# Optimization experiments

Hardware: AMD Instinct MI355X
Metric: run time of the kernel (lower is better)

## Reference

```python
import jax, jax.numpy as jnp
import numpy as np

N, E, F_IN = 100000, 1000000, 128
H, C = 4, 32
HC = H * C
D_DIR = 128
G = 250
HID, CLS = 128, 2
ALPHA = 0.5
NEG = 0.2  # LeakyReLU slope in GATv2


def setup_inputs() -> dict:
    key = jax.random.key(0)
    ks = jax.random.split(key, 16)
    p = lambda k, shape: 0.02 * jax.random.normal(k, shape, jnp.float32)
    return {
        "x": jax.random.normal(ks[0], (N, F_IN), jnp.float32),
        "edge_index": jax.random.randint(ks[1], (2, E), 0, N, dtype=jnp.int32),
        "edge_attr": jax.random.normal(ks[2], (E, 1), jnp.float32),
        "batch": jnp.sort(jax.random.randint(ks[3], (N,), 0, G, dtype=jnp.int32)),
        "dir_w_in": p(ks[4], (2, F_IN, D_DIR)),
        "dir_b_in": jnp.zeros((2, D_DIR), jnp.float32),
        "dir_w_out": p(ks[5], (2, F_IN, D_DIR)),
        "dir_b_out": jnp.zeros((2, D_DIR), jnp.float32),
        "gat_wl": p(ks[6], (F_IN, HC)),
        "gat_wr": p(ks[7], (F_IN, HC)),
        "gat_we": p(ks[8], (1, HC)),
        "gat_att": p(ks[9], (H, C)),
        "gat_b": jnp.zeros((HC,), jnp.float32),
        "w1": p(ks[10], (D_DIR + HC, HID)),
        "b1": jnp.zeros((HID,), jnp.float32),
        "w2": p(ks[11], (HID, CLS)),
        "b2": jnp.zeros((CLS,), jnp.float32),
    }


def _gcn(x, src, dst, W, b):
    # GCNConv with add_self_loops=False (forced by DirGNNConv), unit edge weights.
    deg = jnp.zeros((N,), x.dtype).at[dst].add(1.0)
    dinv = jnp.where(deg > 0, 1.0 / jnp.sqrt(jnp.maximum(deg, 1.0)), 0.0)
    norm = dinv[src] * dinv[dst]  # [E]
    h = x @ W  # [N, D]
    out = jnp.zeros((N, W.shape[1]), x.dtype).at[dst].add(norm[:, None] * h[src])
    return out + b


def _mean_pool(h, batch):
    cnt = jnp.zeros((G,), h.dtype).at[batch].add(1.0)
    s = jnp.zeros((G, h.shape[1]), h.dtype).at[batch].add(h)
    return s / jnp.maximum(cnt, 1.0)[:, None]


def _forward(x, edge_index, edge_attr, batch, dir_w_in, dir_b_in, dir_w_out, dir_b_out,
             gat_wl, gat_wr, gat_we, gat_att, gat_b, w1, b1, w2, b2):
    src, dst = edge_index[0], edge_index[1]
    # --- DirGNN branch: alpha * GCN(flipped edges) + (1-alpha) * GCN(edges), relu between ---
    h = x
    for i in range(2):
        x_in = _gcn(h, src, dst, dir_w_in[i], dir_b_in[i])
        x_out = _gcn(h, dst, src, dir_w_out[i], dir_b_out[i])
        h = jax.nn.relu(ALPHA * x_out + (1.0 - ALPHA) * x_in)
    x1 = _mean_pool(h, batch)  # [G, D_DIR]
    # --- GATv2 branch (self loops appended, edge_attr fill value 1.0) ---
    loop = jnp.arange(N, dtype=src.dtype)
    s2 = jnp.concatenate([src, loop])
    d2 = jnp.concatenate([dst, loop])
    ea = jnp.concatenate([edge_attr, jnp.ones((N, 1), edge_attr.dtype)], axis=0)
    gl = (x @ gat_wl).reshape(N, H, C)  # source transform
    gr = (x @ gat_wr).reshape(N, H, C)  # target transform
    ee = (ea @ gat_we).reshape(-1, H, C)
    e = jax.nn.leaky_relu(gl[s2] + gr[d2] + ee, NEG)  # [E+N, H, C]
    logits = jnp.einsum('ehc,hc->eh', e, gat_att)
    # segment softmax over incoming edges of each target node (self loops => nonempty)
    m = jnp.full((N, H), -jnp.inf, logits.dtype).at[d2].max(logits)
    ex = jnp.exp(logits - m[d2])
    denom = jnp.zeros((N, H), logits.dtype).at[d2].add(ex)
    att = ex / denom[d2]
    out2 = jnp.zeros((N, H, C), x.dtype).at[d2].add(att[:, :, None] * gl[s2])
    x2 = _mean_pool(out2.reshape(N, HC) + gat_b, batch)  # [G, HC]
    # --- head ---
    z = jnp.concatenate([x1, x2], axis=1)
    z = jax.nn.relu(z @ w1 + b1)
    return z @ w2 + b2  # [G, CLS]


def reference(x, edge_index, edge_attr, batch, dir_w_in, dir_b_in, dir_w_out, dir_b_out,
              gat_wl, gat_wr, gat_we, gat_att, gat_b, w1, b1, w2, b2):
    return _forward(x, edge_index, edge_attr, batch, dir_w_in, dir_b_in, dir_w_out, dir_b_out,
                    gat_wl, gat_wr, gat_we, gat_att, gat_b, w1, b1, w2, b2)
```

## Files before the change

kernel.cpp:

```cpp
#include <hip/hip_runtime.h>
#include <cstdint>

#define FDIM 128
#define PCH 64

static inline int cdiv(long long a, long long b) { return (int)((a + b - 1) / b); }

__global__ __launch_bounds__(256) void degi_kernel(const int* __restrict__ src,
                                                   const int* __restrict__ dst,
                                                   int* __restrict__ deg_in,
                                                   int* __restrict__ deg_out, int E) {
  int base = (blockIdx.x * 256 + threadIdx.x) * 2;
  if (base + 2 <= E) {
    int2 s2 = *(const int2*)(src + base);
    int2 d2 = *(const int2*)(dst + base);
    atomicAdd(&deg_in[d2.x], 1);
    atomicAdd(&deg_in[d2.y], 1);
    atomicAdd(&deg_out[s2.x], 1);
    atomicAdd(&deg_out[s2.y], 1);
  } else {
    for (int i = base; i < E; i++) {
      atomicAdd(&deg_in[dst[i]], 1);
      atomicAdd(&deg_out[src[i]], 1);
    }
  }
}

__global__ __launch_bounds__(256) void dinv2_kernel(const int* __restrict__ degs,
                                                    float* __restrict__ dinv, int n2) {
  int i = blockIdx.x * 256 + threadIdx.x;
  if (i < n2) {
    int v = degs[i];
    dinv[i] = v > 0 ? 1.0f / sqrtf((float)v) : 0.f;
  }
}

__global__ __launch_bounds__(256) void cnt_sorted(const int* __restrict__ batch,
                                                  float* __restrict__ cnt, int N, int G) {
  int g = blockIdx.x * 256 + threadIdx.x;
  if (g >= G) return;
  int lo = 0, hi = N;
  while (lo < hi) { int mid = (lo + hi) >> 1; if (batch[mid] < g) lo = mid + 1; else hi = mid; }
  int lo2 = lo, hi2 = N;
  while (lo2 < hi2) { int mid = (lo2 + hi2) >> 1; if (batch[mid] <= g) lo2 = mid + 1; else hi2 = mid; }
  cnt[g] = (float)(lo2 - lo);
}

__global__ __launch_bounds__(256) void scan1(const int* __restrict__ in, int* __restrict__ out,
                                             int* __restrict__ bsums, int n) {
  __shared__ int tmp[256];
  int t = threadIdx.x;
  int base = blockIdx.x * 1024 + t * 4;
  int a[4];
#pragma unroll
  for (int j = 0; j < 4; j++) a[j] = (base + j < n) ? in[base + j] : 0;
  int s = a[0] + a[1] + a[2] + a[3];
  tmp[t] = s;
  __syncthreads();
  for (int off = 1; off < 256; off <<= 1) {
    int v = (t >= off) ? tmp[t - off] : 0;
    __syncthreads();
    tmp[t] += v;
    __syncthreads();
  }
  int excl = tmp[t] - s;
  int run = excl;
#pragma unroll
  for (int j = 0; j < 4; j++) {
    if (base + j < n) out[base + j] = run;
    run += a[j];
  }
  if (t == 255) bsums[blockIdx.x] = tmp[255];
}

__global__ __launch_bounds__(256) void scan2(const int* __restrict__ bsums,
                                             int* __restrict__ boff, int nb) {
  __shared__ int tmp[256];
  int t = threadIdx.x;
  int s = (t < nb) ? bsums[t] : 0;
  tmp[t] = s;
  __syncthreads();
  for (int off = 1; off < 256; off <<= 1) {
    int v = (t >= off) ? tmp[t - off] : 0;
    __syncthreads();
    tmp[t] += v;
    __syncthreads();
  }
  if (t < nb) boff[t] = tmp[t] - s;
}

__global__ __launch_bounds__(256) void scan3(const int* __restrict__ scanned,
                                             const int* __restrict__ boff,
                                             int* __restrict__ rp_in, int* __restrict__ cur_in,
                                             int* __restrict__ rp_out, int* __restrict__ cur_out,
                                             int N, int E, int n2) {
  int i = blockIdx.x * 256 + threadIdx.x;
  if (i < n2) {
    int v = scanned[i] + boff[i >> 10];
    if (i < N) { rp_in[i] = v; cur_in[i] = v; }
    else { v -= E; rp_out[i - N] = v; cur_out[i - N] = v; }
  }
}

__global__ __launch_bounds__(256) void mm0_fill(const float* __restrict__ A,
                                                const float* __restrict__ W0,
                                                const float* __restrict__ W1,
                                                float* __restrict__ out0,
                                                float* __restrict__ out1, int nrows, int mmB,
                                                const int* __restrict__ src,
                                                const int* __restrict__ dst,
                                                const float* __restrict__ eattr,
                                                int* __restrict__ cur_in,
                                                int* __restrict__ cur_out,
                                                int2* __restrict__ csr_in,
                                                int* __restrict__ csr_out_dst, int E, int fillB) {
  __shared__ float As[64][128];
  __shared__ float Ws[64][64];
  int T = mmB + fillB;
  int bid = blockIdx.x;
  int tid = threadIdx.x;
  long long f0 = (long long)bid * fillB / T;
  long long f1 = (long long)(bid + 1) * fillB / T;

  if (f1 > f0) {
    int base = ((int)f0 * 256 + tid) * 4;
    if (base + 4 <= E) {
      int4 s4 = *(const int4*)(src + base);
      int4 d4 = *(const int4*)(dst + base);
      float4 e4 = *(const float4*)(eattr + base);
      int p0 = atomicAdd(&cur_in[d4.x], 1);
      int p1 = atomicAdd(&cur_in[d4.y], 1);
      int p2 = atomicAdd(&cur_in[d4.z], 1);
      int p3 = atomicAdd(&cur_in[d4.w], 1);
      int q0 = atomicAdd(&cur_out[s4.x], 1);
      int q1 = atomicAdd(&cur_out[s4.y], 1);
      int q2 = atomicAdd(&cur_out[s4.z], 1);
      int q3 = atomicAdd(&cur_out[s4.w], 1);
      csr_in[p0] = make_int2(s4.x, __float_as_int(e4.x));
      csr_in[p1] = make_int2(s4.y, __float_as_int(e4.y));
      csr_in[p2] = make_int2(s4.z, __float_as_int(e4.z));
      csr_in[p3] = make_int2(s4.w, __float_as_int(e4.w));
      csr_out_dst[q0] = d4.x;
      csr_out_dst[q1] = d4.y;
      csr_out_dst[q2] = d4.z;
      csr_out_dst[q3] = d4.w;
    } else {
      for (int i = base; i < E; i++) {
        int s = src[i], d = dst[i];
        int p = atomicAdd(&cur_in[d], 1);
        csr_in[p] = make_int2(s, __float_as_int(eattr[i]));
        int q = atomicAdd(&cur_out[s], 1);
        csr_out_dst[q] = d;
      }
    }
    return;
  }

  int mb = bid - (int)f0;
  int r0 = mb * 64;

#pragma unroll
  for (int i = 0; i < 8; i++) {
    int v = tid + 256 * i;
    int r = v >> 5, k4 = (v & 31) << 2;
    int row = r0 + r;
    float4 a;
    if (row < nrows) a = *(const float4*)(A + (size_t)row * FDIM + k4);
    else a = make_float4(0.f, 0.f, 0.f, 0.f);
    int swz = ((r >> 2) & 7) << 2;
    *(float4*)(&As[r][k4 ^ swz]) = a;
  }

  int tx = tid & 15, ty = tid >> 4;
  int rbase = ty * 4;
  int swz = (ty & 7) << 2;

  for (int p = 0; p < 4; p++) {
    const float* W = (p < 2) ? W0 : W1;
    float* out = (p < 2) ? out0 : out1;
    int cb = (p & 1) * 64;
    float acc[4][4] = {};

    for (int kh = 0; kh < 2; kh++) {
      __syncthreads();
#pragma unroll
      for (int i = 0; i < 4; i++) {
        int v = tid + 256 * i;
        int k = v >> 4, c4 = (v & 15) << 2;
        *(float4*)(&Ws[k][c4]) = *(const float4*)(W + (kh * 64 + k) * FDIM + cb + c4);
      }
      __syncthreads();

#pragma unroll 8
      for (int k = 0; k < 64; k++) {
        int kx = (kh * 64 + k) ^ swz;
        float a0 = As[rbase + 0][kx];
        float a1 = As[rbase + 1][kx];
        float a2 = As[rbase + 2][kx];
        float a3 = As[rbase + 3][kx];
        float4 w = *(float4*)(&Ws[k][tx * 4]);
        acc[0][0] += a0 * w.x; acc[0][1] += a0 * w.y; acc[0][2] += a0 * w.z; acc[0][3] += a0 * w.w;
        acc[1][0] += a1 * w.x; acc[1][1] += a1 * w.y; acc[1][2] += a1 * w.z; acc[1][3] += a1 * w.w;
        acc[2][0] += a2 * w.x; acc[2][1] += a2 * w.y; acc[2][2] += a2 * w.z; acc[2][3] += a2 * w.w;
        acc[3][0] += a3 * w.x; acc[3][1] += a3 * w.y; acc[3][2] += a3 * w.z; acc[3][3] += a3 * w.w;
      }
    }

#pragma unroll
    for (int rr = 0; rr < 4; rr++) {
      int row = r0 + rbase + rr;
      if (row < nrows) {
        float4 o = make_float4(acc[rr][0], acc[rr][1], acc[rr][2], acc[rr][3]);
        *(float4*)(out + (size_t)row * FDIM + cb + tx * 4) = o;
      }
    }
  }
}

__global__ __launch_bounds__(256) void mm128d(const float* __restrict__ A,
                                              const float* __restrict__ W0,
                                              const float* __restrict__ W1,
                                              float* __restrict__ out0,
                                              float* __restrict__ out1, int nrows) {
  __shared__ float As[64][128];
  __shared__ float Ws[64][64];
  int r0 = blockIdx.x * 64;
  int tid = threadIdx.x;

#pragma unroll
  for (int i = 0; i < 8; i++) {
    int v = tid + 256 * i;
    int r = v >> 5, k4 = (v & 31) << 2;
    int row = r0 + r;
    float4 a;
    if (row < nrows) a = *(const float4*)(A + (size_t)row * FDIM + k4);
    else a = make_float4(0.f, 0.f, 0.f, 0.f);
    int swz = ((r >> 2) & 7) << 2;
    *(float4*)(&As[r][k4 ^ swz]) = a;
  }

  int tx = tid & 15, ty = tid >> 4;
  int rbase = ty * 4;
  int swz = (ty & 7) << 2;

  for (int p = 0; p < 4; p++) {
    const float* W = (p < 2) ? W0 : W1;
    float* out = (p < 2) ? out0 : out1;
    int cb = (p & 1) * 64;
    float acc[4][4] = {};

    for (int kh = 0; kh < 2; kh++) {
      __syncthreads();
#pragma unroll
      for (int i = 0; i < 4; i++) {
        int v = tid + 256 * i;
        int k = v >> 4, c4 = (v & 15) << 2;
        *(float4*)(&Ws[k][c4]) = *(const float4*)(W + (kh * 64 + k) * FDIM + cb + c4);
      }
      __syncthreads();

#pragma unroll 8
      for (int k = 0; k < 64; k++) {
        int kx = (kh * 64 + k) ^ swz;
        float a0 = As[rbase + 0][kx];
        float a1 = As[rbase + 1][kx];
        float a2 = As[rbase + 2][kx];
        float a3 = As[rbase + 3][kx];
        float4 w = *(float4*)(&Ws[k][tx * 4]);
        acc[0][0] += a0 * w.x; acc[0][1] += a0 * w.y; acc[0][2] += a0 * w.z; acc[0][3] += a0 * w.w;
        acc[1][0] += a1 * w.x; acc[1][1] += a1 * w.y; acc[1][2] += a1 * w.z; acc[1][3] += a1 * w.w;
        acc[2][0] += a2 * w.x; acc[2][1] += a2 * w.y; acc[2][2] += a2 * w.z; acc[2][3] += a2 * w.w;
        acc[3][0] += a3 * w.x; acc[3][1] += a3 * w.y; acc[3][2] += a3 * w.z; acc[3][3] += a3 * w.w;
      }
    }

#pragma unroll
    for (int rr = 0; rr < 4; rr++) {
      int row = r0 + rbase + rr;
      if (row < nrows) {
        float4 o = make_float4(acc[rr][0], acc[rr][1], acc[rr][2], acc[rr][3]);
        *(float4*)(out + (size_t)row * FDIM + cb + tx * 4) = o;
      }
    }
  }
}

__global__ __launch_bounds__(128) void gcn_gather4(const float4* __restrict__ tin,
                                                   const float4* __restrict__ tout,
                                                   const int* __restrict__ rp_in,
                                                   const int* __restrict__ deg_in,
                                                   const int2* __restrict__ adj_in,
                                                   const int* __restrict__ rp_out,
                                                   const int* __restrict__ deg_out,
                                                   const int* __restrict__ adj_out,
                                                   const float* __restrict__ dinv_in,
                                                   const float* __restrict__ dinv_out,
                                                   const float* __restrict__ bin,
                                                   const float* __restrict__ bout,
                                                   float4* __restrict__ outp, int N) {
  int grp = threadIdx.x >> 5, lane = threadIdx.x & 31;
  int d = blockIdx.x * 4 + grp;
  if (d >= N) return;
  float wi = 0.5f * dinv_in[d], wo = 0.5f * dinv_out[d];
  float4 a0 = make_float4(0.f, 0.f, 0.f, 0.f);
  float4 a1 = a0, a2 = a0, a3 = a0;

  int p = rp_in[d], n1 = deg_in[d];
  int k = 0;
  for (; k + 4 <= n1; k += 4) {
    int s0 = adj_in[p + k].x, s1 = adj_in[p + k + 1].x, s2 = adj_in[p + k + 2].x, s3 = adj_in[p + k + 3].x;
    float w0 = wi * dinv_in[s0], w1 = wi * dinv_in[s1], w2 = wi * dinv_in[s2], w3 = wi * dinv_in[s3];
    float4 v0 = tin[(size_t)s0 * 32 + lane];
    float4 v1 = tin[(size_t)s1 * 32 + lane];
    float4 v2 = tin[(size_t)s2 * 32 + lane];
    float4 v3 = tin[(size_t)s3 * 32 + lane];
    a0.x += w0 * v0.x; a0.y += w0 * v0.y; a0.z += w0 * v0.z; a0.w += w0 * v0.w;
    a1.x += w1 * v1.x; a1.y += w1 * v1.y; a1.z += w1 * v1.z; a1.w += w1 * v1.w;
    a2.x += w2 * v2.x; a2.y += w2 * v2.y; a2.z += w2 * v2.z; a2.w += w2 * v2.w;
    a3.x += w3 * v3.x; a3.y += w3 * v3.y; a3.z += w3 * v3.z; a3.w += w3 * v3.w;
  }
  for (; k < n1; k++) {
    int s = adj_in[p + k].x;
    float w = wi * dinv_in[s];
    float4 v = tin[(size_t)s * 32 + lane];
    a0.x += w * v.x; a0.y += w * v.y; a0.z += w * v.z; a0.w += w * v.w;
  }

  int q = rp_out[d], n2 = deg_out[d];
  k = 0;
  for (; k + 4 <= n2; k += 4) {
    int s0 = adj_out[q + k], s1 = adj_out[q + k + 1], s2 = adj_out[q + k + 2], s3 = adj_out[q + k + 3];
    float w0 = wo * dinv_out[s0], w1 = wo * dinv_out[s1], w2 = wo * dinv_out[s2], w3 = wo * dinv_out[s3];
    float4 v0 = tout[(size_t)s0 * 32 + lane];
    float4 v1 = tout[(size_t)s1 * 32 + lane];
    float4 v2 = tout[(size_t)s2 * 32 + lane];
    float4 v3 = tout[(size_t)s3 * 32 + lane];
    a0.x += w0 * v0.x; a0.y += w0 * v0.y; a0.z += w0 * v0.z; a0.w += w0 * v0.w;
    a1.x += w1 * v1.x; a1.y += w1 * v1.y; a1.z += w1 * v1.z; a1.w += w1 * v1.w;
    a2.x += w2 * v2.x; a2.y += w2 * v2.y; a2.z += w2 * v2.z; a2.w += w2 * v2.w;
    a3.x += w3 * v3.x; a3.y += w3 * v3.y; a3.z += w3 * v3.z; a3.w += w3 * v3.w;
  }
  for (; k < n2; k++) {
    int s = adj_out[q + k];
    float w = wo * dinv_out[s];
    float4 v = tout[(size_t)s * 32 + lane];
    a0.x += w * v.x; a0.y += w * v.y; a0.z += w * v.z; a0.w += w * v.w;
  }

  float4 acc;
  acc.x = (a0.x + a1.x) + (a2.x + a3.x);
  acc.y = (a0.y + a1.y) + (a2.y + a3.y);
  acc.z = (a0.z + a1.z) + (a2.z + a3.z);
  acc.w = (a0.w + a1.w) + (a2.w + a3.w);

  const float4* b1 = (const float4*)bin;
  const float4* b2 = (const float4*)bout;
  float4 ba = b1[lane], bb = b2[lane];
  float4 o;
  o.x = acc.x + 0.5f * (ba.x + bb.x);
  o.y = acc.y + 0.5f * (ba.y + bb.y);
  o.z = acc.z + 0.5f * (ba.z + bb.z);
  o.w = acc.w + 0.5f * (ba.w + bb.w);
  o.x = o.x > 0.f ? o.x : 0.f;
  o.y = o.y > 0.f ? o.y : 0.f;
  o.z = o.z > 0.f ? o.z : 0.f;
  o.w = o.w > 0.f ? o.w : 0.f;
  outp[(size_t)d * 32 + lane] = o;
}

__global__ __launch_bounds__(128) void gat_fused2(const float4* __restrict__ gl,
                                                  const float4* __restrict__ gr,
                                                  const int* __restrict__ rp,
                                                  const int* __restrict__ deg,
                                                  const int2* __restrict__ adj,
                                                  const float* __restrict__ we,
                                                  const float* __restrict__ att,
                                                  const float* __restrict__ gatb,
                                                  float4* __restrict__ outp, int N) {
  int grp = threadIdx.x >> 5, lane = threadIdx.x & 31;
  int d = blockIdx.x * 4 + grp;
  if (d >= N) return;

  float4 grv = gr[(size_t)d * 32 + lane];
  float4 wev = ((const float4*)we)[lane];
  float4 atv = ((const float4*)att)[lane];

  int p = rp[d], n1 = deg[d];
  float m = -1e30f, den = 0.f;
  float4 o = make_float4(0.f, 0.f, 0.f, 0.f);

#define GAT_LOGIT(g4, ea, pv)                                                     \
  {                                                                               \
    float vx = g4.x + grv.x + (ea) * wev.x; vx = vx > 0.f ? vx : 0.2f * vx;       \
    float vy = g4.y + grv.y + (ea) * wev.y; vy = vy > 0.f ? vy : 0.2f * vy;       \
    float vz = g4.z + grv.z + (ea) * wev.z; vz = vz > 0.f ? vz : 0.2f * vz;       \
    float vw = g4.w + grv.w + (ea) * wev.w; vw = vw > 0.f ? vw : 0.2f * vw;       \
    pv = vx * atv.x + vy * atv.y + vz * atv.z + vw * atv.w;                       \
    pv += __shfl_xor(pv, 1);                                                      \
    pv += __shfl_xor(pv, 2);                                                      \
    pv += __shfl_xor(pv, 4);                                                      \
  }

#define GAT_UPDATE(g4, pv)                                                        \
  {                                                                               \
    float mn = fmaxf(m, pv);                                                      \
    float sc = expf(m - mn);                                                      \
    float w = expf(pv - mn);                                                      \
    den = den * sc + w;                                                           \
    o.x = o.x * sc + w * g4.x;                                                    \
    o.y = o.y * sc + w * g4.y;                                                    \
    o.z = o.z * sc + w * g4.z;                                                    \
    o.w = o.w * sc + w * g4.w;                                                    \
    m = mn;                                                                       \
  }

  int k = 0;
  for (; k + 2 <= n1; k += 2) {
    int2 e0 = adj[p + k], e1 = adj[p + k + 1];
    int s0 = e0.x, s1 = e1.x;
    float ea0 = __int_as_float(e0.y), ea1 = __int_as_float(e1.y);
    float4 g0 = gl[(size_t)s0 * 32 + lane];
    float4 g1 = gl[(size_t)s1 * 32 + lane];
    float pv0, pv1;
    GAT_LOGIT(g0, ea0, pv0);
    GAT_LOGIT(g1, ea1, pv1);
    GAT_UPDATE(g0, pv0);
    GAT_UPDATE(g1, pv1);
  }
  if (k < n1) {
    int2 e = adj[p + k];
    float ea = __int_as_float(e.y);
    float4 g = gl[(size_t)e.x * 32 + lane];
    float pv;
    GAT_LOGIT(g, ea, pv);
    GAT_UPDATE(g, pv);
  }
  {
    float4 g = gl[(size_t)d * 32 + lane];
    float pv;
    GAT_LOGIT(g, 1.0f, pv);
    GAT_UPDATE(g, pv);
  }
#undef GAT_LOGIT
#undef GAT_UPDATE

  float4 bb = ((const float4*)gatb)[lane];
  float4 r;
  r.x = o.x / den + bb.x;
  r.y = o.y / den + bb.y;
  r.z = o.z / den + bb.z;
  r.w = o.w / den + bb.w;
  outp[(size_t)d * 32 + lane] = r;
}

__global__ __launch_bounds__(128) void pool_kernel(const float* __restrict__ srcf,
                                                   const int* __restrict__ batch,
                                                   float* __restrict__ zb,
                                                   int colOff, int N) {
  __shared__ int sb[PCH];
  int c0 = blockIdx.x * PCH;
  int t = threadIdx.x;
  int nmax = N - c0; if (nmax > PCH) nmax = PCH;
  if (t < nmax) sb[t] = batch[c0 + t];
  __syncthreads();
  float run = 0.f;
  int gp = sb[0];
  for (int i = 0; i < nmax; i++) {
    int g = sb[i];
    if (g != gp) {
      atomicAdd(&zb[(size_t)gp * 256 + colOff + t], run);
      run = 0.f; gp = g;
    }
    run += srcf[(size_t)(c0 + i) * FDIM + t];
  }
  atomicAdd(&zb[(size_t)gp * 256 + colOff + t], run);
}

__global__ __launch_bounds__(128) void head_kernel(const float* __restrict__ zb,
                                                   const float* __restrict__ cnt,
                                                   const float* __restrict__ w1,
                                                   const float* __restrict__ b1,
                                                   const float* __restrict__ w2,
                                                   const float* __restrict__ b2,
                                                   float* __restrict__ out, int G) {
  __shared__ float z[256];
  __shared__ float y[128];
  int g = blockIdx.x, t = threadIdx.x;
  float c = cnt[g];
  float cm = c > 1.f ? c : 1.f;
  z[t]       = zb[(size_t)g * 256 + t] / cm;
  z[t + 128] = zb[(size_t)g * 256 + 128 + t] / cm;
  __syncthreads();
  float acc = b1[t];
  for (int k = 0; k < 256; k++) acc += z[k] * w1[k * 128 + t];
  y[t] = acc > 0.f ? acc : 0.f;
  __syncthreads();
  if (t < 2) {
    float o = b2[t];
    for (int j = 0; j < 128; j++) o += y[j] * w2[j * 2 + t];
    out[(size_t)g * 2 + t] = o;
  }
}

extern "C" void kernel_launch(void* const* d_in, const int* in_sizes, int n_in,
                              void* d_out, int out_size, void* d_ws, size_t ws_size,
                              hipStream_t stream) {
  const float* x     = (const float*)d_in[0];
  const int*   ei    = (const int*)d_in[1];
  const float* eattr = (const float*)d_in[2];
  const int*   batch = (const int*)d_in[3];
  const float* dwi   = (const float*)d_in[4];
  const float* dbi   = (const float*)d_in[5];
  const float* dwo   = (const float*)d_in[6];
  const float* dbo   = (const float*)d_in[7];
  const float* wl    = (const float*)d_in[8];
  const float* wr    = (const float*)d_in[9];
  const float* we    = (const float*)d_in[10];
  const float* att   = (const float*)d_in[11];
  const float* gatb  = (const float*)d_in[12];
  const float* w1    = (const float*)d_in[13];
  const float* b1    = (const float*)d_in[14];
  const float* w2    = (const float*)d_in[15];
  const float* b2    = (const float*)d_in[16];

  int N = in_sizes[0] / FDIM;
  int E = in_sizes[1] / 2;
  int G = out_size / 2;
  const int* src = ei;
  const int* dst = ei + E;

  float* ws = (float*)d_ws;
  size_t off = 0;
  float* A        = ws + off; off += (size_t)N * FDIM;
  float* B        = ws + off; off += (size_t)N * FDIM;
  float* C        = ws + off; off += (size_t)N * FDIM;
  float* dinv2    = ws + off; off += 2 * (size_t)N;
  int* deg2       = (int*)(ws + off); off += 2 * (size_t)N;
  int* rpt        = (int*)(ws + off); off += 2 * (size_t)N;
  int* rp_in      = (int*)(ws + off); off += (size_t)N;
  int* rp_out     = (int*)(ws + off); off += (size_t)N;
  int* cur_in     = (int*)(ws + off); off += (size_t)N;
  int* cur_out    = (int*)(ws + off); off += (size_t)N;
  int2* csr_in    = (int2*)(ws + off); off += 2 * (size_t)E;
  int* csr_out_dst= (int*)(ws + off); off += (size_t)E;
  int* bsums      = (int*)(ws + off); off += 256;
  int* boff       = (int*)(ws + off); off += 256;
  float* zb       = ws + off; off += (size_t)G * 256;
  float* cnt      = ws + off; off += (size_t)G;

  int* deg_in = deg2, *deg_out = deg2 + N;
  float* dinv_in = dinv2, *dinv_out = dinv2 + N;

  int n2 = 2 * N;
  int nb1 = cdiv(n2, 1024);

  hipMemsetAsync(deg2, 0, (size_t)n2 * sizeof(int), stream);
  degi_kernel<<<cdiv(E, 512), 256, 0, stream>>>(src, dst, deg_in, deg_out, E);
  dinv2_kernel<<<cdiv((long long)n2, 256), 256, 0, stream>>>(deg2, dinv2, n2);
  scan1<<<nb1, 256, 0, stream>>>(deg2, rpt, bsums, n2);
  scan2<<<1, 256, 0, stream>>>(bsums, boff, nb1);
  scan3<<<cdiv(n2, 256), 256, 0, stream>>>(rpt, boff, rp_in, cur_in, rp_out, cur_out, N, E, n2);

  hipMemsetAsync(zb, 0, (size_t)G * 256 * sizeof(float), stream);
  cnt_sorted<<<cdiv(G, 256), 256, 0, stream>>>(batch, cnt, N, G);

  int mmB = cdiv(N, 64);
  int fillB = cdiv(E, 1024);
  mm0_fill<<<mmB + fillB, 256, 0, stream>>>(x, dwi, dwo, B, C, N, mmB,
                                            src, dst, eattr, cur_in, cur_out,
                                            csr_in, csr_out_dst, E, fillB);

  gcn_gather4<<<cdiv(N, 4), 128, 0, stream>>>((const float4*)B, (const float4*)C,
                                              rp_in, deg_in, csr_in,
                                              rp_out, deg_out, csr_out_dst,
                                              dinv_in, dinv_out, dbi, dbo, (float4*)A, N);
  mm128d<<<mmB, 256, 0, stream>>>(A, dwi + 16384, dwo + 16384, B, C, N);
  gcn_gather4<<<cdiv(N, 4), 128, 0, stream>>>((const float4*)B, (const float4*)C,
                                              rp_in, deg_in, csr_in,
                                              rp_out, deg_out, csr_out_dst,
                                              dinv_in, dinv_out, dbi + 128, dbo + 128, (float4*)A, N);
  pool_kernel<<<cdiv(N, PCH), 128, 0, stream>>>(A, batch, zb, 0, N);

  mm128d<<<mmB, 256, 0, stream>>>(x, wl, wr, B, C, N);
  gat_fused2<<<cdiv(N, 4), 128, 0, stream>>>((const float4*)B, (const float4*)C,
                                             rp_in, deg_in, csr_in,
                                             we, att, gatb, (float4*)A, N);
  pool_kernel<<<cdiv(N, PCH), 128, 0, stream>>>(A, batch, zb, 128, N);

  head_kernel<<<G, 128, 0, stream>>>(zb, cnt, w1, b1, w2, b2, (float*)d_out, G);
}
```

Before: 1.082 ms.

## Co-schedule independent matmuls with gathers in fused kernels and fuse pooling atomics

Merges the independent GAT projection matmul into the first GCN gather launch, and the second DirGNN matmul into the GAT attention launch. Blocks are interleaved between matmul and gather roles so compute-bound and memory-bound work share the GPU. The GAT and second GCN gathers now accumulate straight into pooled sums with atomics, which removes the intermediate writes and the pool_kernel passes. This needs two extra N×128 workspace buffers, uses a smaller 32-row matmul tile, and adds float atomic contention on 250 graph rows; a fallback path keeps the old sequence when workspace is short.

```diff
diff --git a/kernel.cpp b/kernel.cpp
--- a/kernel.cpp
+++ b/kernel.cpp
@@ -101,6 +101,216 @@
     else { v -= E; rp_out[i - N] = v; cur_out[i - N] = v; }
   }
 }
+
+
+__device__ __forceinline__ float4 gcn_node_val(int d, int lane,
+    const float4* __restrict__ tin, const float4* __restrict__ tout,
+    const int* __restrict__ rp_in, const int* __restrict__ deg_in, const int2* __restrict__ adj_in,
+    const int* __restrict__ rp_out, const int* __restrict__ deg_out, const int* __restrict__ adj_out,
+    const float* __restrict__ dinv_in, const float* __restrict__ dinv_out,
+    const float* __restrict__ bin, const float* __restrict__ bout) {
+  float wi = 0.5f * dinv_in[d], wo = 0.5f * dinv_out[d];
+  float4 a0 = make_float4(0.f, 0.f, 0.f, 0.f);
+  float4 a1 = a0, a2 = a0, a3 = a0;
+
+  int p = rp_in[d], n1 = deg_in[d];
+  int k = 0;
+  for (; k + 4 <= n1; k += 4) {
+    int s0 = adj_in[p + k].x, s1 = adj_in[p + k + 1].x, s2 = adj_in[p + k + 2].x, s3 = adj_in[p + k + 3].x;
+    float w0 = wi * dinv_in[s0], w1 = wi * dinv_in[s1], w2 = wi * dinv_in[s2], w3 = wi * dinv_in[s3];
+    float4 v0 = tin[(size_t)s0 * 32 + lane];
+    float4 v1 = tin[(size_t)s1 * 32 + lane];
+    float4 v2 = tin[(size_t)s2 * 32 + lane];
+    float4 v3 = tin[(size_t)s3 * 32 + lane];
+    a0.x += w0 * v0.x; a0.y += w0 * v0.y; a0.z += w0 * v0.z; a0.w += w0 * v0.w;
+    a1.x += w1 * v1.x; a1.y += w1 * v1.y; a1.z += w1 * v1.z; a1.w += w1 * v1.w;
+    a2.x += w2 * v2.x; a2.y += w2 * v2.y; a2.z += w2 * v2.z; a2.w += w2 * v2.w;
+    a3.x += w3 * v3.x; a3.y += w3 * v3.y; a3.z += w3 * v3.z; a3.w += w3 * v3.w;
+  }
+  for (; k < n1; k++) {
+    int s = adj_in[p + k].x;
+    float w = wi * dinv_in[s];
+    float4 v = tin[(size_t)s * 32 + lane];
+    a0.x += w * v.x; a0.y += w * v.y; a0.z += w * v.z; a0.w += w * v.w;
+  }
+
+  int q = rp_out[d], n2 = deg_out[d];
+  k = 0;
+  for (; k + 4 <= n2; k += 4) {
+    int s0 = adj_out[q + k], s1 = adj_out[q + k + 1], s2 = adj_out[q + k + 2], s3 = adj_out[q + k + 3];
+    float w0 = wo * dinv_out[s0], w1 = wo * dinv_out[s1], w2 = wo * dinv_out[s2], w3 = wo * dinv_out[s3];
+    float4 v0 = tout[(size_t)s0 * 32 + lane];
+    float4 v1 = tout[(size_t)s1 * 32 + lane];
+    float4 v2 = tout[(size_t)s2 * 32 + lane];
+    float4 v3 = tout[(size_t)s3 * 32 + lane];
+    a0.x += w0 * v0.x; a0.y += w0 * v0.y; a0.z += w0 * v0.z; a0.w += w0 * v0.w;
+    a1.x += w1 * v1.x; a1.y += w1 * v1.y; a1.z += w1 * v1.z; a1.w += w1 * v1.w;
+    a2.x += w2 * v2.x; a2.y += w2 * v2.y; a2.z += w2 * v2.z; a2.w += w2 * v2.w;
+    a3.x += w3 * v3.x; a3.y += w3 * v3.y; a3.z += w3 * v3.z; a3.w += w3 * v3.w;
+  }
+  for (; k < n2; k++) {
+    int s = adj_out[q + k];
+    float w = wo * dinv_out[s];
+    float4 v = tout[(size_t)s * 32 + lane];
+    a0.x += w * v.x; a0.y += w * v.y; a0.z += w * v.z; a0.w += w * v.w;
+  }
+
+  float4 acc;
+  acc.x = (a0.x + a1.x) + (a2.x + a3.x);
+  acc.y = (a0.y + a1.y) + (a2.y + a3.y);
+  acc.z = (a0.z + a1.z) + (a2.z + a3.z);
+  acc.w = (a0.w + a1.w) + (a2.w + a3.w);
+
+  float4 ba = ((const float4*)bin)[lane], bb = ((const float4*)bout)[lane];
+  float4 o;
+  o.x = acc.x + 0.5f * (ba.x + bb.x);
+  o.y = acc.y + 0.5f * (ba.y + bb.y);
+  o.z = acc.z + 0.5f * (ba.z + bb.z);
+  o.w = acc.w + 0.5f * (ba.w + bb.w);
+  o.x = o.x > 0.f ? o.x : 0.f;
+  o.y = o.y > 0.f ? o.y : 0.f;
+  o.z = o.z > 0.f ? o.z : 0.f;
+  o.w = o.w > 0.f ? o.w : 0.f;
+  return o;
+}
+
+__device__ __forceinline__ float4 gat_node_val(int d, int lane,
+    const float4* __restrict__ gl, const float4* __restrict__ gr,
+    const int* __restrict__ rp, const int* __restrict__ deg, const int2* __restrict__ adj,
+    const float* __restrict__ we, const float* __restrict__ att,
+    const float* __restrict__ gatb) {
+  float4 grv = gr[(size_t)d * 32 + lane];
+  float4 wev = ((const float4*)we)[lane];
+  float4 atv = ((const float4*)att)[lane];
+
+  int p = rp[d], n1 = deg[d];
+  float m = -1e30f, den = 0.f;
+  float4 o = make_float4(0.f, 0.f, 0.f, 0.f);
+
+#define GAT_LOGIT(g4, ea, pv)                                                     \
+  {                                                                               \
+    float vx = g4.x + grv.x + (ea) * wev.x; vx = vx > 0.f ? vx : 0.2f * vx;       \
+    float vy = g4.y + grv.y + (ea) * wev.y; vy = vy > 0.f ? vy : 0.2f * vy;       \
+    float vz = g4.z + grv.z + (ea) * wev.z; vz = vz > 0.f ? vz : 0.2f * vz;       \
+    float vw = g4.w + grv.w + (ea) * wev.w; vw = vw > 0.f ? vw : 0.2f * vw;       \
+    pv = vx * atv.x + vy * atv.y + vz * atv.z + vw * atv.w;                       \
+    pv += __shfl_xor(pv, 1);                                                      \
+    pv += __shfl_xor(pv, 2);                                                      \
+    pv += __shfl_xor(pv, 4);                                                      \
+  }
+
+#define GAT_UPDATE(g4, pv)                                                        \
+  {                                                                               \
+    float mn = fmaxf(m, pv);                                                      \
+    float sc = expf(m - mn);                                                      \
+    float w = expf(pv - mn);                                                      \
+    den = den * sc + w;                                                           \
+    o.x = o.x * sc + w * g4.x;                                                    \
+    o.y = o.y * sc + w * g4.y;                                                    \
+    o.z = o.z * sc + w * g4.z;                                                    \
+    o.w = o.w * sc + w * g4.w;                                                    \
+    m = mn;                                                                       \
+  }
+
+  int k = 0;
+  for (; k + 2 <= n1; k += 2) {
+    int2 e0 = adj[p + k], e1 = adj[p + k + 1];
+    float ea0 = __int_as_float(e0.y), ea1 = __int_as_float(e1.y);
+    float4 g0 = gl[(size_t)e0.x * 32 + lane];
+    float4 g1 = gl[(size_t)e1.x * 32 + lane];
+    float pv0, pv1;
+    GAT_LOGIT(g0, ea0, pv0);
+    GAT_LOGIT(g1, ea1, pv1);
+    GAT_UPDATE(g0, pv0);
+    GAT_UPDATE(g1, pv1);
+  }
+  if (k < n1) {
+    int2 e = adj[p + k];
+    float ea = __int_as_float(e.y);
+    float4 g = gl[(size_t)e.x * 32 + lane];
+    float pv;
+    GAT_LOGIT(g, ea, pv);
+    GAT_UPDATE(g, pv);
+  }
+  {
+    float4 g = gl[(size_t)d * 32 + lane];
+    float pv;
+    GAT_LOGIT(g, 1.0f, pv);
+    GAT_UPDATE(g, pv);
+  }
+#undef GAT_LOGIT
+#undef GAT_UPDATE
+
+  float4 bb = ((const float4*)gatb)[lane];
+  float4 r;
+  r.x = o.x / den + bb.x;
+  r.y = o.y / den + bb.y;
+  r.z = o.z / den + bb.z;
+  r.w = o.w / den + bb.w;
+  return r;
+}
+
+__device__ __forceinline__ void mm32_dual(const float* __restrict__ A,
+                                          const float* __restrict__ W0,
+                                          const float* __restrict__ W1,
+                                          float* __restrict__ out0,
+                                          float* __restrict__ out1,
+                                          int nrows, int r0, int tid,
+                                          float (*As)[128], float (*Ws)[64]) {
+#pragma unroll
+  for (int i = 0; i < 4; i++) {
+    int v = tid + 256 * i;
+    int r = v >> 5, k4 = (v & 31) << 2;
+    int row = r0 + r;
+    float4 a;
+    if (row < nrows) a = *(const float4*)(A + (size_t)row * FDIM + k4);
+    else a = make_float4(0.f, 0.f, 0.f, 0.f);
+    int swz = ((r >> 2) & 7) << 2;
+    *(float4*)(&As[r][k4 ^ swz]) = a;
+  }
+
+  int tx = tid & 15, ty = tid >> 4;
+  int rbase = ty * 2;
+  int swz = ((ty >> 1) & 7) << 2;
+
+  for (int p = 0; p < 4; p++) {
+    const float* W = (p < 2) ? W0 : W1;
+    float* out = (p < 2) ? out0 : out1;
+    int cb = (p & 1) * 64;
+    float acc[2][4] = {};
+
+    for (int kh = 0; kh < 2; kh++) {
+      __syncthreads();
+#pragma unroll
+      for (int i = 0; i < 4; i++) {
+        int v = tid + 256 * i;
+        int k = v >> 4, c4 = (v & 15) << 2;
+        *(float4*)(&Ws[k][c4]) = *(const float4*)(W + (kh * 64 + k) * FDIM + cb + c4);
+      }
+      __syncthreads();
+
+#pragma unroll 8
+      for (int k = 0; k < 64; k++) {
+        int kx = (kh * 64 + k) ^ swz;
+        float a0 = As[rbase + 0][kx];
+        float a1 = As[rbase + 1][kx];
+        float4 w = *(float4*)(&Ws[k][tx * 4]);
+        acc[0][0] += a0 * w.x; acc[0][1] += a0 * w.y; acc[0][2] += a0 * w.z; acc[0][3] += a0 * w.w;
+        acc[1][0] += a1 * w.x; acc[1][1] += a1 * w.y; acc[1][2] += a1 * w.z; acc[1][3] += a1 * w.w;
+      }
+    }
+
+#pragma unroll
+    for (int rr = 0; rr < 2; rr++) {
+      int row = r0 + rbase + rr;
+      if (row < nrows) {
+        float4 o = make_float4(acc[rr][0], acc[rr][1], acc[rr][2], acc[rr][3]);
+        *(float4*)(out + (size_t)row * FDIM + cb + tx * 4) = o;
+      }
+    }
+  }
+}
+
 
 __global__ __launch_bounds__(256) void mm0_fill(const float* __restrict__ A,
                                                 const float* __restrict__ W0,
@@ -217,6 +427,85 @@
   }
 }
 
+__global__ __launch_bounds__(256) void gath_mm(
+    const float4* __restrict__ tin, const float4* __restrict__ tout,
+    const int* __restrict__ rp_in, const int* __restrict__ deg_in, const int2* __restrict__ adj_in,
+    const int* __restrict__ rp_out, const int* __restrict__ deg_out, const int* __restrict__ adj_out,
+    const float* __restrict__ dinv_in, const float* __restrict__ dinv_out,
+    const float* __restrict__ bin, const float* __restrict__ bout,
+    float4* __restrict__ outp, int N, int gB,
+    const float* __restrict__ x, const float* __restrict__ wl, const float* __restrict__ wr,
+    float* __restrict__ D, float* __restrict__ Eo, int mB) {
+  __shared__ float As[32][128];
+  __shared__ float Ws[64][64];
+  int T = gB + mB;
+  int bid = blockIdx.x, tid = threadIdx.x;
+  long long m0 = (long long)bid * mB / T;
+  long long m1 = (long long)(bid + 1) * mB / T;
+  if (m1 > m0) {
+    mm32_dual(x, wl, wr, D, Eo, N, (int)m0 * 32, tid, As, Ws);
+    return;
+  }
+  int gbid = bid - (int)m0;
+  int grp = tid >> 5, lane = tid & 31;
+  int d = gbid * 8 + grp;
+  if (d >= N) return;
+  float4 o = gcn_node_val(d, lane, tin, tout, rp_in, deg_in, adj_in,
+                          rp_out, deg_out, adj_out, dinv_in, dinv_out, bin, bout);
+  outp[(size_t)d * 32 + lane] = o;
+}
+
+__global__ __launch_bounds__(256) void mm_gat(
+    const float* __restrict__ A, const float* __restrict__ W0, const float* __restrict__ W1,
+    float* __restrict__ out0, float* __restrict__ out1, int N, int mB,
+    const float4* __restrict__ gl, const float4* __restrict__ gr,
+    const int* __restrict__ rp, const int* __restrict__ deg, const int2* __restrict__ adj,
+    const float* __restrict__ we, const float* __restrict__ att, const float* __restrict__ gatb,
+    const int* __restrict__ batch, float* __restrict__ zb, int gatB) {
+  __shared__ float As[32][128];
+  __shared__ float Ws[64][64];
+  int T = gatB + mB;
+  int bid = blockIdx.x, tid = threadIdx.x;
+  long long m0 = (long long)bid * mB / T;
+  long long m1 = (long long)(bid + 1) * mB / T;
+  if (m1 > m0) {
+    mm32_dual(A, W0, W1, out0, out1, N, (int)m0 * 32, tid, As, Ws);
+    return;
+  }
+  int gbid = bid - (int)m0;
+  int grp = tid >> 5, lane = tid & 31;
+  int d = gbid * 8 + grp;
+  if (d >= N) return;
+  float4 r = gat_node_val(d, lane, gl, gr, rp, deg, adj, we, att, gatb);
+  int g = batch[d];
+  float* dst = &zb[(size_t)g * 256 + 128 + lane * 4];
+  atomicAdd(dst + 0, r.x);
+  atomicAdd(dst + 1, r.y);
+  atomicAdd(dst + 2, r.z);
+  atomicAdd(dst + 3, r.w);
+}
+
+__global__ __launch_bounds__(128) void gcn_gather_pool(
+    const float4* __restrict__ tin, const float4* __restrict__ tout,
+    const int* __restrict__ rp_in, const int* __restrict__ deg_in, const int2* __restrict__ adj_in,
+    const int* __restrict__ rp_out, const int* __restrict__ deg_out, const int* __restrict__ adj_out,
+    const float* __restrict__ dinv_in, const float* __restrict__ dinv_out,
+    const float* __restrict__ bin, const float* __restrict__ bout,
+    const int* __restrict__ batch, float* __restrict__ zb, int N) {
+  int grp = threadIdx.x >> 5, lane = threadIdx.x & 31;
+  int d = blockIdx.x * 4 + grp;
+  if (d >= N) return;
+  float4 o = gcn_node_val(d, lane, tin, tout, rp_in, deg_in, adj_in,
+                          rp_out, deg_out, adj_out, dinv_in, dinv_out, bin, bout);
+  int g = batch[d];
+  float* dst = &zb[(size_t)g * 256 + lane * 4];
+  atomicAdd(dst + 0, o.x);
+  atomicAdd(dst + 1, o.y);
+  atomicAdd(dst + 2, o.z);
+  atomicAdd(dst + 3, o.w);
+}
+
+
 __global__ __launch_bounds__(256) void mm128d(const float* __restrict__ A,
                                               const float* __restrict__ W0,
                                               const float* __restrict__ W1,
@@ -301,70 +590,8 @@
   int grp = threadIdx.x >> 5, lane = threadIdx.x & 31;
   int d = blockIdx.x * 4 + grp;
   if (d >= N) return;
-  float wi = 0.5f * dinv_in[d], wo = 0.5f * dinv_out[d];
-  float4 a0 = make_float4(0.f, 0.f, 0.f, 0.f);
-  float4 a1 = a0, a2 = a0, a3 = a0;
-
-  int p = rp_in[d], n1 = deg_in[d];
-  int k = 0;
-  for (; k + 4 <= n1; k += 4) {
-    int s0 = adj_in[p + k].x, s1 = adj_in[p + k + 1].x, s2 = adj_in[p + k + 2].x, s3 = adj_in[p + k + 3].x;
-    float w0 = wi * dinv_in[s0], w1 = wi * dinv_in[s1], w2 = wi * dinv_in[s2], w3 = wi * dinv_in[s3];
-    float4 v0 = tin[(size_t)s0 * 32 + lane];
-    float4 v1 = tin[(size_t)s1 * 32 + lane];
-    float4 v2 = tin[(size_t)s2 * 32 + lane];
-    float4 v3 = tin[(size_t)s3 * 32 + lane];
-    a0.x += w0 * v0.x; a0.y += w0 * v0.y; a0.z += w0 * v0.z; a0.w += w0 * v0.w;
-    a1.x += w1 * v1.x; a1.y += w1 * v1.y; a1.z += w1 * v1.z; a1.w += w1 * v1.w;
-    a2.x += w2 * v2.x; a2.y += w2 * v2.y; a2.z += w2 * v2.z; a2.w += w2 * v2.w;
-    a3.x += w3 * v3.x; a3.y += w3 * v3.y; a3.z += w3 * v3.z; a3.w += w3 * v3.w;
-  }
-  for (; k < n1; k++) {
-    int s = adj_in[p + k].x;
-    float w = wi * dinv_in[s];
-    float4 v = tin[(size_t)s * 32 + lane];
-    a0.x += w * v.x; a0.y += w * v.y; a0.z += w * v.z; a0.w += w * v.w;
-  }
-
-  int q = rp_out[d], n2 = deg_out[d];
-  k = 0;
-  for (; k + 4 <= n2; k += 4) {
-    int s0 = adj_out[q + k], s1 = adj_out[q + k + 1], s2 = adj_out[q + k + 2], s3 = adj_out[q + k + 3];
-    float w0 = wo * dinv_out[s0], w1 = wo * dinv_out[s1], w2 = wo * dinv_out[s2], w3 = wo * dinv_out[s3];
-    float4 v0 = tout[(size_t)s0 * 32 + lane];
-    float4 v1 = tout[(size_t)s1 * 32 + lane];
-    float4 v2 = tout[(size_t)s2 * 32 + lane];
-    float4 v3 = tout[(size_t)s3 * 32 + lane];
-    a0.x += w0 * v0.x; a0.y += w0 * v0.y; a0.z += w0 * v0.z; a0.w += w0 * v0.w;
-    a1.x += w1 * v1.x; a1.y += w1 * v1.y; a1.z += w1 * v1.z; a1.w += w1 * v1.w;
-    a2.x += w2 * v2.x; a2.y += w2 * v2.y; a2.z += w2 * v2.z; a2.w += w2 * v2.w;
-    a3.x += w3 * v3.x; a3.y += w3 * v3.y; a3.z += w3 * v3.z; a3.w += w3 * v3.w;
-  }
-  for (; k < n2; k++) {
-    int s = adj_out[q + k];
-    float w = wo * dinv_out[s];
-    float4 v = tout[(size_t)s * 32 + lane];
-    a0.x += w * v.x; a0.y += w * v.y; a0.z += w * v.z; a0.w += w * v.w;
-  }
-
-  float4 acc;
-  acc.x = (a0.x + a1.x) + (a2.x + a3.x);
-  acc.y = (a0.y + a1.y) + (a2.y + a3.y);
-  acc.z = (a0.z + a1.z) + (a2.z + a3.z);
-  acc.w = (a0.w + a1.w) + (a2.w + a3.w);
-
-  const float4* b1 = (const float4*)bin;
-  const float4* b2 = (const float4*)bout;
-  float4 ba = b1[lane], bb = b2[lane];
-  float4 o;
-  o.x = acc.x + 0.5f * (ba.x + bb.x);
-  o.y = acc.y + 0.5f * (ba.y + bb.y);
-  o.z = acc.z + 0.5f * (ba.z + bb.z);
-  o.w = acc.w + 0.5f * (ba.w + bb.w);
-  o.x = o.x > 0.f ? o.x : 0.f;
-  o.y = o.y > 0.f ? o.y : 0.f;
-  o.z = o.z > 0.f ? o.z : 0.f;
-  o.w = o.w > 0.f ? o.w : 0.f;
+  float4 o = gcn_node_val(d, lane, tin, tout, rp_in, deg_in, adj_in,
+                          rp_out, deg_out, adj_out, dinv_in, dinv_out, bin, bout);
   outp[(size_t)d * 32 + lane] = o;
 }
 
@@ -380,76 +607,7 @@
   int grp = threadIdx.x >> 5, lane = threadIdx.x & 31;
   int d = blockIdx.x * 4 + grp;
   if (d >= N) return;
-
-  float4 grv = gr[(size_t)d * 32 + lane];
-  float4 wev = ((const float4*)we)[lane];
-  float4 atv = ((const float4*)att)[lane];
-
-  int p = rp[d], n1 = deg[d];
-  float m = -1e30f, den = 0.f;
-  float4 o = make_float4(0.f, 0.f, 0.f, 0.f);
-
-#define GAT_LOGIT(g4, ea, pv)                                                     \
-  {                                                                               \
-    float vx = g4.x + grv.x + (ea) * wev.x; vx = vx > 0.f ? vx : 0.2f * vx;       \
-    float vy = g4.y + grv.y + (ea) * wev.y; vy = vy > 0.f ? vy : 0.2f * vy;       \
-    float vz = g4.z + grv.z + (ea) * wev.z; vz = vz > 0.f ? vz : 0.2f * vz;       \
-    float vw = g4.w + grv.w + (ea) * wev.w; vw = vw > 0.f ? vw : 0.2f * vw;       \
-    pv = vx * atv.x + vy * atv.y + vz * atv.z + vw * atv.w;                       \
-    pv += __shfl_xor(pv, 1);                                                      \
-    pv += __shfl_xor(pv, 2);                                                      \
-    pv += __shfl_xor(pv, 4);                                                      \
-  }
-
-#define GAT_UPDATE(g4, pv)                                                        \
-  {                                                                               \
-    float mn = fmaxf(m, pv);                                                      \
-    float sc = expf(m - mn);                                                      \
-    float w = expf(pv - mn);                                                      \
-    den = den * sc + w;                                                           \
-    o.x = o.x * sc + w * g4.x;                                                    \
-    o.y = o.y * sc + w * g4.y;                                                    \
-    o.z = o.z * sc + w * g4.z;                                                    \
-    o.w = o.w * sc + w * g4.w;                                                    \
-    m = mn;                                                                       \
-  }
-
-  int k = 0;
-  for (; k + 2 <= n1; k += 2) {
-    int2 e0 = adj[p + k], e1 = adj[p + k + 1];
-    int s0 = e0.x, s1 = e1.x;
-    float ea0 = __int_as_float(e0.y), ea1 = __int_as_float(e1.y);
-    float4 g0 = gl[(size_t)s0 * 32 + lane];
-    float4 g1 = gl[(size_t)s1 * 32 + lane];
-    float pv0, pv1;
-    GAT_LOGIT(g0, ea0, pv0);
-    GAT_LOGIT(g1, ea1, pv1);
-    GAT_UPDATE(g0, pv0);
-    GAT_UPDATE(g1, pv1);
-  }
-  if (k < n1) {
-    int2 e = adj[p + k];
-    float ea = __int_as_float(e.y);
-    float4 g = gl[(size_t)e.x * 32 + lane];
-    float pv;
-    GAT_LOGIT(g, ea, pv);
-    GAT_UPDATE(g, pv);
-  }
-  {
-    float4 g = gl[(size_t)d * 32 + lane];
-    float pv;
-    GAT_LOGIT(g, 1.0f, pv);
-    GAT_UPDATE(g, pv);
-  }
-#undef GAT_LOGIT
-#undef GAT_UPDATE
-
-  float4 bb = ((const float4*)gatb)[lane];
-  float4 r;
-  r.x = o.x / den + bb.x;
-  r.y = o.y / den + bb.y;
-  r.z = o.z / den + bb.z;
-  r.w = o.w / den + bb.w;
+  float4 r = gat_node_val(d, lane, gl, gr, rp, deg, adj, we, att, gatb);
   outp[(size_t)d * 32 + lane] = r;
 }
 
@@ -529,11 +687,17 @@
   const int* src = ei;
   const int* dst = ei + E;
 
+  size_t nf = (size_t)N * FDIM;
+  size_t fixed = 10 * (size_t)N + 3 * (size_t)E + 512 + (size_t)G * 257;
+  bool main_path = ((5 * nf + fixed) * sizeof(float)) <= ws_size;
+
   float* ws = (float*)d_ws;
   size_t off = 0;
-  float* A        = ws + off; off += (size_t)N * FDIM;
-  float* B        = ws + off; off += (size_t)N * FDIM;
-  float* C        = ws + off; off += (size_t)N * FDIM;
+  float* A = ws + off; off += nf;
+  float* B = ws + off; off += nf;
+  float* C = ws + off; off += nf;
+  float* D = nullptr; float* Eb = nullptr;
+  if (main_path) { D = ws + off; off += nf; Eb = ws + off; off += nf; }
   float* dinv2    = ws + off; off += 2 * (size_t)N;
   int* deg2       = (int*)(ws + off); off += 2 * (size_t)N;
   int* rpt        = (int*)(ws + off); off += 2 * (size_t)N;
@@ -553,6 +717,8 @@
 
   int n2 = 2 * N;
   int nb1 = cdiv(n2, 1024);
+  int mmB = cdiv(N, 64);
+  int fillB = cdiv(E, 1024);
 
   hipMemsetAsync(deg2, 0, (size_t)n2 * sizeof(int), stream);
   degi_kernel<<<cdiv(E, 512), 256, 0, stream>>>(src, dst, deg_in, deg_out, E);
@@ -564,28 +730,45 @@
   hipMemsetAsync(zb, 0, (size_t)G * 256 * sizeof(float), stream);
   cnt_sorted<<<cdiv(G, 256), 256, 0, stream>>>(batch, cnt, N, G);
 
-  int mmB = cdiv(N, 64);
-  int fillB = cdiv(E, 1024);
   mm0_fill<<<mmB + fillB, 256, 0, stream>>>(x, dwi, dwo, B, C, N, mmB,
                                             src, dst, eattr, cur_in, cur_out,
                                             csr_in, csr_out_dst, E, fillB);
 
-  gcn_gather4<<<cdiv(N, 4), 128, 0, stream>>>((const float4*)B, (const float4*)C,
-                                              rp_in, deg_in, csr_in,
-                                              rp_out, deg_out, csr_out_dst,
-                                              dinv_in, dinv_out, dbi, dbo, (float4*)A, N);
-  mm128d<<<mmB, 256, 0, stream>>>(A, dwi + 16384, dwo + 16384, B, C, N);
-  gcn_gather4<<<cdiv(N, 4), 128, 0, stream>>>((const float4*)B, (const float4*)C,
-                                              rp_in, deg_in, csr_in,
-                                              rp_out, deg_out, csr_out_dst,
-                                              dinv_in, dinv_out, dbi + 128, dbo + 128, (float4*)A, N);
-  pool_kernel<<<cdiv(N, PCH), 128, 0, stream>>>(A, batch, zb, 0, N);
-
-  mm128d<<<mmB, 256, 0, stream>>>(x, wl, wr, B, C, N);
-  gat_fused2<<<cdiv(N, 4), 128, 0, stream>>>((const float4*)B, (const float4*)C,
-                                             rp_in, deg_in, csr_in,
-                                             we, att, gatb, (float4*)A, N);
-  pool_kernel<<<cdiv(N, PCH), 128, 0, stream>>>(A, batch, zb, 128, N);
+  if (main_path) {
+    int gB = cdiv(N, 8);
+    int m32B = cdiv(N, 32);
+    gath_mm<<<gB + m32B, 256, 0, stream>>>((const float4*)B, (const float4*)C,
+                                           rp_in, deg_in, csr_in,
+                                           rp_out, deg_out, csr_out_dst,
+                                           dinv_in, dinv_out, dbi, dbo,
+                                           (float4*)A, N, gB,
+                                           x, wl, wr, D, Eb, m32B);
+    mm_gat<<<gB + m32B, 256, 0, stream>>>(A, dwi + 16384, dwo + 16384, B, C, N, m32B,
+                                          (const float4*)D, (const float4*)Eb,
+                                          rp_in, deg_in, csr_in,
+                                          we, att, gatb, batch, zb, gB);
+    gcn_gather_pool<<<cdiv(N, 4), 128, 0, stream>>>((const float4*)B, (const float4*)C,
+                                                    rp_in, deg_in, csr_in,
+                                                    rp_out, deg_out, csr_out_dst,
+                                                    dinv_in, dinv_out, dbi + 128, dbo + 128,
+                                                    batch, zb, N);
+  } else {
+    gcn_gather4<<<cdiv(N, 4), 128, 0, stream>>>((const float4*)B, (const float4*)C,
+                                                rp_in, deg_in, csr_in,
+                                                rp_out, deg_out, csr_out_dst,
+                                                dinv_in, dinv_out, dbi, dbo, (float4*)A, N);
+    mm128d<<<mmB, 256, 0, stream>>>(A, dwi + 16384, dwo + 16384, B, C, N);
+    gcn_gather4<<<cdiv(N, 4), 128, 0, stream>>>((const float4*)B, (const float4*)C,
+                                                rp_in, deg_in, csr_in,
+                                                rp_out, deg_out, csr_out_dst,
+                                                dinv_in, dinv_out, dbi + 128, dbo + 128, (float4*)A, N);
+    pool_kernel<<<cdiv(N, PCH), 128, 0, stream>>>(A, batch, zb, 0, N);
+    mm128d<<<mmB, 256, 0, stream>>>(x, wl, wr, B, C, N);
+    gat_fused2<<<cdiv(N, 4), 128, 0, stream>>>((const float4*)B, (const float4*)C,
+                                               rp_in, deg_in, csr_in,
+                                               we, att, gatb, (float4*)A, N);
+    pool_kernel<<<cdiv(N, PCH), 128, 0, stream>>>(A, batch, zb, 128, N);
+  }
 
   head_kernel<<<G, 128, 0, stream>>>(zb, cnt, w1, b1, w2, b2, (float*)d_out, G);
 }
```

Measured after the change: 1.080 ms. About the same (-0.2%).
